# Kernel tuning notes

Measured on AMD Instinct MI355X. Metric: run time of the kernel, lower is better.

## Reference

```python
import jax, jax.numpy as jnp
import numpy as np

B, T, D, H = 128, 2048, 512, 8
HD = D // H  # head_dim = 64

def setup_inputs() -> dict:
    key = jax.random.key(0)
    ks = jax.random.split(key, 8)
    x = jax.random.normal(ks[0], (B, T, D), dtype=jnp.float32)
    mask_bool = jax.random.randint(ks[1], (B, T), 0, 2) > 0
    temp = jnp.ones((H,), dtype=jnp.float32)
    w_sal = jax.random.normal(ks[2], (D, H), dtype=jnp.float32) * (1.0 / np.sqrt(D))
    b_sal = jnp.zeros((H,), dtype=jnp.float32)
    w_gate = jax.random.normal(ks[3], (HD, 1), dtype=jnp.float32) * (1.0 / np.sqrt(HD))
    b_gate = jnp.zeros((1,), dtype=jnp.float32)
    scale = jnp.ones((D,), dtype=jnp.float32)
    return {"x": x, "mask_bool": mask_bool, "temp": temp, "w_sal": w_sal,
            "b_sal": b_sal, "w_gate": w_gate, "b_gate": b_gate, "scale": scale}

def reference(x, mask_bool, temp, w_sal, b_sal, w_gate, b_gate, scale):
    Bx, Tx, Dx = x.shape
    x_heads = x.reshape(Bx, Tx, H, HD)
    temperature = jax.nn.softplus(temp) + 0.3              # [H]
    logits = (jnp.einsum('btd,dh->bth', x, w_sal) + b_sal) / temperature[None, None, :]
    m = mask_bool[:, :, None]                              # [B,T,1]
    safe_logits = jnp.where(m, logits, -1e9)
    max_logits = jax.lax.stop_gradient(jnp.max(safe_logits, axis=1, keepdims=True))
    exps = jnp.where(m, jnp.exp(safe_logits - max_logits), 0.0)
    weights = exps / (jnp.sum(exps, axis=1, keepdims=True) + 1e-6)  # [B,T,H]
    write_vec_heads = jnp.einsum('bth,bthd->bhd', weights, x_heads)  # [B,H,HD]
    gate_logits = jnp.einsum('bhd,do->bho', write_vec_heads, w_gate) + b_gate  # [B,H,1]
    window_valid = jnp.any(mask_bool, axis=1)[:, None, None]
    write_u_heads = jax.nn.sigmoid(gate_logits) * window_valid.astype(jnp.float32)  # [B,H,1]
    write_vec = write_vec_heads.reshape(Bx, Dx)
    rms = jnp.sqrt(jnp.mean(jnp.square(write_vec), axis=-1, keepdims=True) + 1e-6)
    write_vec = write_vec / rms * scale
    write_u_expanded = jnp.tile(write_u_heads, (1, 1, HD)).reshape(Bx, Dx)
    return (write_vec, write_u_expanded, write_u_heads.squeeze(-1))
```

## Files before the change

kernel.cpp:

```cpp
#include <hip/hip_runtime.h>

#define B_DIM 128
#define T_DIM 2048
#define D_DIM 512
#define H_DIM 8
#define HD_DIM 64
#define CH 4
#define ROWS_PER_BLOCK (T_DIM / CH)
#define WAVES 8
#define ROWS_PER_WAVE (ROWS_PER_BLOCK / WAVES)

typedef float f4v __attribute__((ext_vector_type(4)));

#define ROW_BODY(ROW, B0, B1)                                                  \
  {                                                                            \
    const int row_ = (ROW);                                                    \
    float p0 = B0.x * w[0];                                                    \
    float p1 = B0.x * w[1];                                                    \
    float p2 = B0.x * w[2];                                                    \
    float p3 = B0.x * w[3];                                                    \
    float p4 = B0.x * w[4];                                                    \
    float p5 = B0.x * w[5];                                                    \
    float p6 = B0.x * w[6];                                                    \
    float p7 = B0.x * w[7];                                                    \
    p0 = fmaf(B0.y, w[8+0], p0);  p1 = fmaf(B0.y, w[8+1], p1);                 \
    p2 = fmaf(B0.y, w[8+2], p2);  p3 = fmaf(B0.y, w[8+3], p3);                 \
    p4 = fmaf(B0.y, w[8+4], p4);  p5 = fmaf(B0.y, w[8+5], p5);                 \
    p6 = fmaf(B0.y, w[8+6], p6);  p7 = fmaf(B0.y, w[8+7], p7);                 \
    p0 = fmaf(B0.z, w[16+0], p0); p1 = fmaf(B0.z, w[16+1], p1);                \
    p2 = fmaf(B0.z, w[16+2], p2); p3 = fmaf(B0.z, w[16+3], p3);                \
    p4 = fmaf(B0.z, w[16+4], p4); p5 = fmaf(B0.z, w[16+5], p5);                \
    p6 = fmaf(B0.z, w[16+6], p6); p7 = fmaf(B0.z, w[16+7], p7);                \
    p0 = fmaf(B0.w, w[24+0], p0); p1 = fmaf(B0.w, w[24+1], p1);                \
    p2 = fmaf(B0.w, w[24+2], p2); p3 = fmaf(B0.w, w[24+3], p3);                \
    p4 = fmaf(B0.w, w[24+4], p4); p5 = fmaf(B0.w, w[24+5], p5);                \
    p6 = fmaf(B0.w, w[24+6], p6); p7 = fmaf(B0.w, w[24+7], p7);                \
    p0 = fmaf(B1.x, w[32+0], p0); p1 = fmaf(B1.x, w[32+1], p1);                \
    p2 = fmaf(B1.x, w[32+2], p2); p3 = fmaf(B1.x, w[32+3], p3);                \
    p4 = fmaf(B1.x, w[32+4], p4); p5 = fmaf(B1.x, w[32+5], p5);                \
    p6 = fmaf(B1.x, w[32+6], p6); p7 = fmaf(B1.x, w[32+7], p7);                \
    p0 = fmaf(B1.y, w[40+0], p0); p1 = fmaf(B1.y, w[40+1], p1);                \
    p2 = fmaf(B1.y, w[40+2], p2); p3 = fmaf(B1.y, w[40+3], p3);                \
    p4 = fmaf(B1.y, w[40+4], p4); p5 = fmaf(B1.y, w[40+5], p5);                \
    p6 = fmaf(B1.y, w[40+6], p6); p7 = fmaf(B1.y, w[40+7], p7);                \
    p0 = fmaf(B1.z, w[48+0], p0); p1 = fmaf(B1.z, w[48+1], p1);                \
    p2 = fmaf(B1.z, w[48+2], p2); p3 = fmaf(B1.z, w[48+3], p3);                \
    p4 = fmaf(B1.z, w[48+4], p4); p5 = fmaf(B1.z, w[48+5], p5);                \
    p6 = fmaf(B1.z, w[48+6], p6); p7 = fmaf(B1.z, w[48+7], p7);                \
    p0 = fmaf(B1.w, w[56+0], p0); p1 = fmaf(B1.w, w[56+1], p1);                \
    p2 = fmaf(B1.w, w[56+2], p2); p3 = fmaf(B1.w, w[56+3], p3);                \
    p4 = fmaf(B1.w, w[56+4], p4); p5 = fmaf(B1.w, w[56+5], p5);                \
    p6 = fmaf(B1.w, w[56+6], p6); p7 = fmaf(B1.w, w[56+7], p7);                \
    const bool hi5 = (lane & 32) != 0;                         \
    float q0 = (hi5 ? p2 : p0) + __shfl_xor(hi5 ? p0 : p2, 32, 64);            \
    float q1 = (hi5 ? p3 : p1) + __shfl_xor(hi5 ? p1 : p3, 32, 64);            \
    float q2 = (hi5 ? p6 : p4) + __shfl_xor(hi5 ? p4 : p6, 32, 64);            \
    float q3 = (hi5 ? p7 : p5) + __shfl_xor(hi5 ? p5 : p7, 32, 64);            \
    const bool hi4 = (lane & 16) != 0;                         \
    float sA = (hi4 ? q1 : q0) + __shfl_xor(hi4 ? q0 : q1, 16, 64);            \
    float sB = (hi4 ? q3 : q2) + __shfl_xor(hi4 ? q2 : q3, 16, 64);            \
    sA += __shfl_xor(sA, 8, 64);  sB += __shfl_xor(sB, 8, 64);                 \
    sA += __shfl_xor(sA, 4, 64);  sB += __shfl_xor(sB, 4, 64);                 \
    sA += __shfl_xor(sA, 2, 64);  sB += __shfl_xor(sB, 2, 64);                 \
    sA += __shfl_xor(sA, 1, 64);  sB += __shfl_xor(sB, 1, 64);                 \
    const bool valid = (rowmask >> row_) & 1ull;                               \
    const float lgA = valid ? (sA + bsA) * invTA : -1e9f;                      \
    const float lgB = valid ? (sB + bsB) * invTB : -1e9f;                      \
    const bool needA = lgA > mA + 8.0f;                                        \
    const bool needB = lgB > mB + 8.0f;                                        \
    if (__any(needA || needB)) {                                               \
      const float mnA = needA ? lgA : mA;                                      \
      const float scA = __expf(mA - mnA);                                      \
      const float mnB = needB ? lgB : mB;                                      \
      const float scB = __expf(mB - mnB);                                      \
      lA *= scA; lB *= scB;                                                    \
      acc0 *= scA; acc1 *= scA; acc2 *= scA; acc3 *= scA;                      \
      acc4 *= scB; acc5 *= scB; acc6 *= scB; acc7 *= scB;                      \
      mA = mnA; mB = mnB;                                                      \
    }                                                                          \
    const float peA = valid ? __expf(lgA - mA) : 0.0f;                         \
    const float peB = valid ? __expf(lgB - mB) : 0.0f;                         \
    lA += peA; lB += peB;                                                      \
    acc0 = fmaf(peA, B0.x, acc0); acc1 = fmaf(peA, B0.y, acc1);                \
    acc2 = fmaf(peA, B0.z, acc2); acc3 = fmaf(peA, B0.w, acc3);                \
    acc4 = fmaf(peB, B1.x, acc4); acc5 = fmaf(peB, B1.y, acc5);                \
    acc6 = fmaf(peB, B1.z, acc6); acc7 = fmaf(peB, B1.w, acc7);                \
    const int pr_ = (row_ + 2 < ROWS_PER_WAVE) ? (row_ + 2)                    \
                                               : (ROWS_PER_WAVE - 1);          \
    const f4v* pp_ = xb + (size_t)pr_ * (D_DIM / 4);                           \
    B0 = pp_[0];                                                               \
    B1 = pp_[64];                                                              \
  }

__global__ __launch_bounds__(512, 4) void salience_pass1(
    const float* __restrict__ x,
    const void* __restrict__ mask,
    const float* __restrict__ temp,
    const float* __restrict__ w_sal,
    const float* __restrict__ b_sal,
    float* __restrict__ ws_hm,
    float* __restrict__ ws_hl,
    float* __restrict__ ws_hacc)
{
    __shared__ float sm_acc[WAVES][D_DIM];
    __shared__ float sm_m[WAVES][H_DIM];
    __shared__ float sm_l[WAVES][H_DIM];

    const int b     = blockIdx.x >> 2;
    const int chunk = blockIdx.x & 3;
    const int lane  = threadIdx.x & 63;
    const int wv    = threadIdx.x >> 6;
    const int hA    = lane >> 4;

    const unsigned mv0 = (unsigned)((const int*)mask)[lane];
    const int byte_mask = (__ballot(mv0 > 1u) != 0ull) ? 1 : 0;

    float w[64];
    {
        const float4* wa = (const float4*)(w_sal) + (size_t)lane * 8;
        const float4* wb = (const float4*)(w_sal + 2048) + (size_t)lane * 8;
        #pragma unroll
        for (int q = 0; q < 8; ++q) {
            float4 v = wa[q];
            w[q*4+0] = v.x; w[q*4+1] = v.y; w[q*4+2] = v.z; w[q*4+3] = v.w;
        }
        #pragma unroll
        for (int q = 0; q < 8; ++q) {
            float4 v = wb[q];
            w[32+q*4+0] = v.x; w[32+q*4+1] = v.y; w[32+q*4+2] = v.z; w[32+q*4+3] = v.w;
        }
    }
    const float bsA = b_sal[hA];
    const float bsB = b_sal[hA + 4];
    const float tpA = temp[hA];
    const float tpB = temp[hA + 4];
    const float spA = (tpA > 20.0f) ? tpA : log1pf(__expf(tpA));
    const float spB = (tpB > 20.0f) ? tpB : log1pf(__expf(tpB));
    const float invTA = 1.0f / (spA + 0.3f);
    const float invTB = 1.0f / (spB + 0.3f);

    const int t0 = chunk * ROWS_PER_BLOCK + wv * ROWS_PER_WAVE;
    const size_t mbase = (size_t)b * T_DIM + t0;

    int mrow = byte_mask ? (int)((const unsigned char*)mask)[mbase + lane]
                         : ((const int*)mask)[mbase + lane];
    const unsigned long long rowmask = __ballot(mrow != 0);

    float mA = -1e9f, lA = 0.0f;
    float mB = -1e9f, lB = 0.0f;
    float acc0 = 0.f, acc1 = 0.f, acc2 = 0.f, acc3 = 0.f;
    float acc4 = 0.f, acc5 = 0.f, acc6 = 0.f, acc7 = 0.f;

    const f4v* xb = (const f4v*)(x + ((size_t)b * T_DIM + t0) * D_DIM) + lane;

    f4v bA0 = xb[0];
    f4v bA1 = xb[64];
    f4v bB0 = xb[128];
    f4v bB1 = xb[192];

    for (int r2 = 0; r2 < ROWS_PER_WAVE / 2; ++r2) {
        ROW_BODY(2 * r2,     bA0, bA1)
        ROW_BODY(2 * r2 + 1, bB0, bB1)
    }

    if ((lane & 15) == 0) {
        sm_m[wv][hA]     = mA;
        sm_m[wv][hA + 4] = mB;
        sm_l[wv][hA]     = lA;
        sm_l[wv][hA + 4] = lB;
    }
    float4* dstA = (float4*)(&sm_acc[wv][0]) + lane;
    dstA[0]  = make_float4(acc0, acc1, acc2, acc3);
    dstA[64] = make_float4(acc4, acc5, acc6, acc7);
    __syncthreads();

    const int d = threadIdx.x;
    const int h = d >> 6;
    float M = -3.0e38f;
    #pragma unroll
    for (int s = 0; s < WAVES; ++s) M = fmaxf(M, sm_m[s][h]);
    float A = 0.0f, L = 0.0f;
    #pragma unroll
    for (int s = 0; s < WAVES; ++s) {
        const float e = __expf(sm_m[s][h] - M);
        L = fmaf(sm_l[s][h], e, L);
        A = fmaf(sm_acc[s][d], e, A);
    }
    const size_t hc = (size_t)b * CH + chunk;
    ws_hacc[hc * D_DIM + d] = A;
    if ((d & 63) == 0) {
        ws_hm[hc * H_DIM + h] = M;
        ws_hl[hc * H_DIM + h] = L;
    }
}

__global__ __launch_bounds__(512) void salience_pass2(
    const float* __restrict__ ws_hm,
    const float* __restrict__ ws_hl,
    const float* __restrict__ ws_hacc,
    const float* __restrict__ w_gate,
    const float* __restrict__ b_gate,
    const float* __restrict__ scale,
    float* __restrict__ out)
{
    const int b  = blockIdx.x;
    const int d  = threadIdx.x;
    const int h  = d >> 6;
    const int dd = d & 63;

    __shared__ float red[H_DIM];

    const size_t h0 = (size_t)b * CH;
    const float m0 = ws_hm[(h0 + 0) * H_DIM + h];
    const float m1 = ws_hm[(h0 + 1) * H_DIM + h];
    const float m2 = ws_hm[(h0 + 2) * H_DIM + h];
    const float m3 = ws_hm[(h0 + 3) * H_DIM + h];
    const float M  = fmaxf(fmaxf(m0, m1), fmaxf(m2, m3));
    const float e0 = __expf(m0 - M);
    const float e1 = __expf(m1 - M);
    const float e2 = __expf(m2 - M);
    const float e3 = __expf(m3 - M);
    const float L = ws_hl[(h0 + 0) * H_DIM + h] * e0
                  + ws_hl[(h0 + 1) * H_DIM + h] * e1
                  + ws_hl[(h0 + 2) * H_DIM + h] * e2
                  + ws_hl[(h0 + 3) * H_DIM + h] * e3;
    const float A = ws_hacc[(h0 + 0) * D_DIM + d] * e0
                  + ws_hacc[(h0 + 1) * D_DIM + d] * e1
                  + ws_hacc[(h0 + 2) * D_DIM + d] * e2
                  + ws_hacc[(h0 + 3) * D_DIM + d] * e3;
    const float wv = A / (L + 1e-6f);

    float g = wv * w_gate[dd];
    #pragma unroll
    for (int s = 1; s < 64; s <<= 1) g += __shfl_xor(g, s, 64);
    const float gl = g + b_gate[0];
    const float u = (L > 0.0f) ? (1.0f / (1.0f + __expf(-gl))) : 0.0f;

    float sq = wv * wv;
    #pragma unroll
    for (int s = 1; s < 64; s <<= 1) sq += __shfl_xor(sq, s, 64);
    if (dd == 0) red[h] = sq;
    __syncthreads();
    float ssum = 0.0f;
    #pragma unroll
    for (int k = 0; k < H_DIM; ++k) ssum += red[k];
    const float rms = sqrtf(ssum * (1.0f / (float)D_DIM) + 1e-6f);

    out[(size_t)b * D_DIM + d] = wv / rms * scale[d];
    out[(size_t)B_DIM * D_DIM + (size_t)b * D_DIM + d] = u;
    if (dd == 0) out[2 * (size_t)B_DIM * D_DIM + (size_t)b * H_DIM + h] = u;
}

extern "C" void kernel_launch(void* const* d_in, const int* in_sizes, int n_in,
                              void* d_out, int out_size, void* d_ws, size_t ws_size,
                              hipStream_t stream) {
    (void)in_sizes; (void)n_in; (void)out_size; (void)ws_size;
    const float* x      = (const float*)d_in[0];
    const void*  mask   = d_in[1];
    const float* temp   = (const float*)d_in[2];
    const float* w_sal  = (const float*)d_in[3];
    const float* b_sal  = (const float*)d_in[4];
    const float* w_gate = (const float*)d_in[5];
    const float* b_gate = (const float*)d_in[6];
    const float* scale  = (const float*)d_in[7];
    float* out = (float*)d_out;

    char* ws = (char*)d_ws;
    float* ws_hm   = (float*)(ws);
    float* ws_hl   = (float*)(ws + 16384);
    float* ws_hacc = (float*)(ws + 32768);

    salience_pass1<<<B_DIM * CH, WAVES * 64, 0, stream>>>(
        x, mask, temp, w_sal, b_sal, ws_hm, ws_hl, ws_hacc);
    salience_pass2<<<B_DIM, 512, 0, stream>>>(
        ws_hm, ws_hl, ws_hacc, w_gate, b_gate, scale, out);
}
```

Before: 113.2 us.

## Fuse two-pass salience kernels via last-block atomic counter finalization

```diff
diff --git a/kernel.cpp b/kernel.cpp
--- a/kernel.cpp
+++ b/kernel.cpp
@@ -92,19 +92,26 @@
     B1 = pp_[64];                                                              \
   }
 
-__global__ __launch_bounds__(512, 4) void salience_pass1(
+__global__ __launch_bounds__(512, 4) void salience_fused(
     const float* __restrict__ x,
     const void* __restrict__ mask,
     const float* __restrict__ temp,
     const float* __restrict__ w_sal,
     const float* __restrict__ b_sal,
+    const float* __restrict__ w_gate,
+    const float* __restrict__ b_gate,
+    const float* __restrict__ scale,
+    int* __restrict__ ws_cnt,
     float* __restrict__ ws_hm,
     float* __restrict__ ws_hl,
-    float* __restrict__ ws_hacc)
+    float* __restrict__ ws_hacc,
+    float* __restrict__ out)
 {
     __shared__ float sm_acc[WAVES][D_DIM];
     __shared__ float sm_m[WAVES][H_DIM];
     __shared__ float sm_l[WAVES][H_DIM];
+    __shared__ float red[H_DIM];
+    __shared__ int   sm_last;
 
     const int b     = blockIdx.x >> 2;
     const int chunk = blockIdx.x & 3;
@@ -176,40 +183,35 @@
 
     const int d = threadIdx.x;
     const int h = d >> 6;
-    float M = -3.0e38f;
-    #pragma unroll
-    for (int s = 0; s < WAVES; ++s) M = fmaxf(M, sm_m[s][h]);
-    float A = 0.0f, L = 0.0f;
-    #pragma unroll
-    for (int s = 0; s < WAVES; ++s) {
-        const float e = __expf(sm_m[s][h] - M);
-        L = fmaf(sm_l[s][h], e, L);
-        A = fmaf(sm_acc[s][d], e, A);
-    }
-    const size_t hc = (size_t)b * CH + chunk;
-    ws_hacc[hc * D_DIM + d] = A;
-    if ((d & 63) == 0) {
-        ws_hm[hc * H_DIM + h] = M;
-        ws_hl[hc * H_DIM + h] = L;
-    }
-}
-
-__global__ __launch_bounds__(512) void salience_pass2(
-    const float* __restrict__ ws_hm,
-    const float* __restrict__ ws_hl,
-    const float* __restrict__ ws_hacc,
-    const float* __restrict__ w_gate,
-    const float* __restrict__ b_gate,
-    const float* __restrict__ scale,
-    float* __restrict__ out)
-{
-    const int b  = blockIdx.x;
-    const int d  = threadIdx.x;
-    const int h  = d >> 6;
+    {
+        float M = -3.0e38f;
+        #pragma unroll
+        for (int s = 0; s < WAVES; ++s) M = fmaxf(M, sm_m[s][h]);
+        float A = 0.0f, L = 0.0f;
+        #pragma unroll
+        for (int s = 0; s < WAVES; ++s) {
+            const float e = __expf(sm_m[s][h] - M);
+            L = fmaf(sm_l[s][h], e, L);
+            A = fmaf(sm_acc[s][d], e, A);
+        }
+        const size_t hc = (size_t)b * CH + chunk;
+        ws_hacc[hc * D_DIM + d] = A;
+        if ((d & 63) == 0) {
+            ws_hm[hc * H_DIM + h] = M;
+            ws_hl[hc * H_DIM + h] = L;
+        }
+    }
+
+    __syncthreads();
+    if (threadIdx.x == 0) {
+        const int old = __hip_atomic_fetch_add(&ws_cnt[b], 1, __ATOMIC_ACQ_REL,
+                                               __HIP_MEMORY_SCOPE_AGENT);
+        sm_last = (old == CH - 1) ? 1 : 0;
+    }
+    __syncthreads();
+    if (!sm_last) return;
+
     const int dd = d & 63;
-
-    __shared__ float red[H_DIM];
-
     const size_t h0 = (size_t)b * CH;
     const float m0 = ws_hm[(h0 + 0) * H_DIM + h];
     const float m1 = ws_hm[(h0 + 1) * H_DIM + h];
@@ -228,15 +230,15 @@
                   + ws_hacc[(h0 + 1) * D_DIM + d] * e1
                   + ws_hacc[(h0 + 2) * D_DIM + d] * e2
                   + ws_hacc[(h0 + 3) * D_DIM + d] * e3;
-    const float wv = A / (L + 1e-6f);
-
-    float g = wv * w_gate[dd];
+    const float wvv = A / (L + 1e-6f);
+
+    float g = wvv * w_gate[dd];
     #pragma unroll
     for (int s = 1; s < 64; s <<= 1) g += __shfl_xor(g, s, 64);
     const float gl = g + b_gate[0];
     const float u = (L > 0.0f) ? (1.0f / (1.0f + __expf(-gl))) : 0.0f;
 
-    float sq = wv * wv;
+    float sq = wvv * wvv;
     #pragma unroll
     for (int s = 1; s < 64; s <<= 1) sq += __shfl_xor(sq, s, 64);
     if (dd == 0) red[h] = sq;
@@ -246,7 +248,7 @@
     for (int k = 0; k < H_DIM; ++k) ssum += red[k];
     const float rms = sqrtf(ssum * (1.0f / (float)D_DIM) + 1e-6f);
 
-    out[(size_t)b * D_DIM + d] = wv / rms * scale[d];
+    out[(size_t)b * D_DIM + d] = wvv / rms * scale[d];
     out[(size_t)B_DIM * D_DIM + (size_t)b * D_DIM + d] = u;
     if (dd == 0) out[2 * (size_t)B_DIM * D_DIM + (size_t)b * H_DIM + h] = u;
 }
@@ -266,12 +268,13 @@
     float* out = (float*)d_out;
 
     char* ws = (char*)d_ws;
-    float* ws_hm   = (float*)(ws);
-    float* ws_hl   = (float*)(ws + 16384);
-    float* ws_hacc = (float*)(ws + 32768);
-
-    salience_pass1<<<B_DIM * CH, WAVES * 64, 0, stream>>>(
-        x, mask, temp, w_sal, b_sal, ws_hm, ws_hl, ws_hacc);
-    salience_pass2<<<B_DIM, 512, 0, stream>>>(
-        ws_hm, ws_hl, ws_hacc, w_gate, b_gate, scale, out);
+    int*   ws_cnt  = (int*)ws;
+    float* ws_hm   = (float*)(ws + 1024);
+    float* ws_hl   = (float*)(ws + 1024 + 16384);
+    float* ws_hacc = (float*)(ws + 1024 + 32768);
+
+    hipMemsetAsync(ws_cnt, 0, B_DIM * sizeof(int), stream);
+    salience_fused<<<B_DIM * CH, WAVES * 64, 0, stream>>>(
+        x, mask, temp, w_sal, b_sal, w_gate, b_gate, scale,
+        ws_cnt, ws_hm, ws_hl, ws_hacc, out);
 }
```

Result: slower. 138.6 us (+22.5%).
